# Optimization experiments

Hardware: AMD Instinct MI355X
Metric: run time of the kernel (lower is better)

The kernel has to match this reference:

```python
import jax, jax.numpy as jnp
import numpy as np

KER = 8

def _gelu(x):
    return jax.nn.gelu(x, approximate=False)

def _conv3x3(x, w, b):
    y = jax.lax.conv_general_dilated(x, w, (1, 1), 'SAME',
                                     dimension_numbers=('NCHW', 'OIHW', 'NCHW'))
    return y + b[None, :, None, None]

def _unfold(x):
    # F.unfold(kernel=8, stride=8): [B,C,H,W] -> [B, C*64, L], C-major then kh,kw
    B, C, H, W = x.shape
    Hb, Wb = H // KER, W // KER
    p = x.reshape(B, C, Hb, KER, Wb, KER).transpose(0, 1, 3, 5, 2, 4)
    return p.reshape(B, C * KER * KER, Hb * Wb)

def _fold(cols, H, W):
    # inverse of _unfold (non-overlapping patches)
    B, CK, L = cols.shape
    C = CK // (KER * KER)
    Hb, Wb = H // KER, W // KER
    p = cols.reshape(B, C, KER, KER, Hb, Wb).transpose(0, 1, 4, 2, 5, 3)
    return p.reshape(B, C, H, W)

def _bn(x, g, b, eps=1e-5):
    # train-mode BatchNorm1d on [B, C, L]: stats over (B, L) per channel
    m = x.mean(axis=(0, 2), keepdims=True)
    v = x.var(axis=(0, 2), keepdims=True)
    return (x - m) * jax.lax.rsqrt(v + eps) * g[None, :, None] + b[None, :, None]


def setup_inputs() -> dict:
    key = jax.random.key(0)
    ks = jax.random.split(key, 10)
    ind, d, hid = 64, 1024, 256
    f = lambda k, s: jax.random.normal(k, s, dtype=jnp.float32) * 0.02
    return {
        'feat': jax.random.normal(ks[0], (4, ind, 256, 256), dtype=jnp.float32),
        'w_enc': f(ks[1], (ind, ind, 3, 3)), 'b_enc': jnp.zeros((ind,), jnp.float32),
        'w_k': f(ks[2], (ind, ind, 3, 3)), 'b_k': jnp.zeros((ind,), jnp.float32),
        'w_v': f(ks[3], (ind, ind, 3, 3)), 'b_v': jnp.zeros((ind,), jnp.float32),
        'fcq_w': f(ks[4], (d, ind * KER * KER)), 'fcq_b': jnp.zeros((d,), jnp.float32),
        'fck_w': f(ks[5], (d, ind * KER * KER)), 'fck_b': jnp.zeros((d,), jnp.float32),
        'bnq_g': jnp.ones((d,), jnp.float32), 'bnq_b': jnp.zeros((d,), jnp.float32),
        'bnk_g': jnp.ones((d,), jnp.float32), 'bnk_b': jnp.zeros((d,), jnp.float32),
        'ff1_w': f(ks[6], (hid, ind)), 'ff1_b': jnp.zeros((hid,), jnp.float32),
        'ff2_w': f(ks[7], (ind, hid)), 'ff2_b': jnp.zeros((ind,), jnp.float32),
    }


def reference(feat, w_enc, b_enc, w_k, b_k, w_v, b_v,
              fcq_w, fcq_b, fck_w, fck_b, bnq_g, bnq_b, bnk_g, bnk_b,
              ff1_w, ff1_b, ff2_w, ff2_b):
    B, C, H, W = feat.shape
    fk = _gelu(_conv3x3(feat, w_k, b_k))
    fv = _gelu(_conv3x3(feat, w_v, b_v))
    refer = _gelu(_conv3x3(feat, w_enc, b_enc))
    q_un = _unfold(refer).transpose(0, 2, 1)   # [B, L, C*64]
    k_un = _unfold(fk).transpose(0, 2, 1)
    v_un = _unfold(fv).transpose(0, 2, 1)
    q = jnp.einsum('blc,dc->bld', q_un, fcq_w) + fcq_b
    q = _bn(q.transpose(0, 2, 1), bnq_g, bnq_b).transpose(0, 2, 1)  # [B, L, 1024]
    k = jnp.einsum('blc,dc->bld', k_un, fck_w) + fck_b
    k = _bn(k.transpose(0, 2, 1), bnk_g, bnk_b).transpose(0, 2, 1)
    scores = jnp.einsum('bld,bmd->blm', q, k) / jnp.sqrt(jnp.float32(q.shape[2]))
    attn = jax.nn.softmax(scores, axis=2)
    out = jnp.einsum('blm,bmc->blc', attn, v_un).transpose(0, 2, 1)  # [B, C*64, L]
    out = _fold(out, H, W)
    h = _gelu(jnp.einsum('bchw,oc->bohw', out, ff1_w) + ff1_b[None, :, None, None])
    h = _gelu(jnp.einsum('bchw,oc->bohw', h, ff2_w) + ff2_b[None, :, None, None])
    return h + feat
```

## Files before the change

### kernel.cpp

```cpp
#include <hip/hip_runtime.h>

typedef unsigned short u16;
typedef float f4 __attribute__((ext_vector_type(4)));
typedef float f32x4 __attribute__((ext_vector_type(4)));
typedef short bf16x8 __attribute__((ext_vector_type(8)));
typedef u16 u16x8 __attribute__((ext_vector_type(8)));
typedef u16 u16x4 __attribute__((ext_vector_type(4)));

__device__ __forceinline__ u16 f2bf(float f){
  unsigned u = __float_as_uint(f);
  u = (u + 0x7FFFu + ((u>>16)&1u)) >> 16;
  return (u16)u;
}
__device__ __forceinline__ float bf2f(u16 u){
  return __uint_as_float(((unsigned)u)<<16);
}
__device__ __forceinline__ float gelu_f(float x){
  float y = 1.5957691216057308f*(x + 0.044715f*x*x*x);
  y = fminf(y, 30.0f);
  float t = __expf(y);
  float r = __builtin_amdgcn_rcpf(t + 1.0f);
  return 0.5f*x*(1.0f + (t - 1.0f)*r);
}

typedef __attribute__((address_space(1))) const unsigned int as1_cuint;
typedef __attribute__((address_space(3))) unsigned int as3_uint;
__device__ __forceinline__ void gload_lds16(const void* g, void* l){
  __builtin_amdgcn_global_load_lds((as1_cuint*)g, (as3_uint*)l, 16, 0, 0);
}

__global__ __launch_bounds__(256) void to_nhwc(
    const float* __restrict__ F, u16* __restrict__ O)
{
  __shared__ float tile[64][65];
  const int t = threadIdx.x, b = blockIdx.y;
  const long px0 = (long)blockIdx.x*64;
  const float* Fb = F + (long)b*64*65536;
  #pragma unroll
  for (int i = 0; i < 4; ++i){
    const int ch = (t>>4) + i*16;
    const int pxo = (t&15)*4;
    f4 v = *(const f4*)&Fb[(long)ch*65536 + px0 + pxo];
    tile[ch][pxo]=v[0]; tile[ch][pxo+1]=v[1]; tile[ch][pxo+2]=v[2]; tile[ch][pxo+3]=v[3];
  }
  __syncthreads();
  const int px = t & 63, ch0 = (t>>6)*16;
  u16x8 o0, o1;
  #pragma unroll
  for (int j = 0; j < 8; ++j){ o0[j]=f2bf(tile[ch0+j][px]); o1[j]=f2bf(tile[ch0+8+j][px]); }
  u16* Ob = O + ((long)b*65536 + px0 + px)*64 + ch0;
  *(u16x8*)Ob = o0; *(u16x8*)(Ob+8) = o1;
}

__global__ __launch_bounds__(256) void wt_prep(
    const float* __restrict__ we, const float* __restrict__ wk,
    const float* __restrict__ wv, u16* __restrict__ Wt2)
{
  const int i = blockIdx.x*256 + threadIdx.x;
  const int cio = i & 31;
  const int t1 = i >> 5;
  const int n  = t1 % 192;
  const int t2 = t1 / 192;
  const int kc = t2 & 1, p = t2 >> 1;
  const int dy = p/3, dx = p - dy*3;
  const int ci = kc*32 + cio;
  const float* W = (n < 64) ? we : (n < 128) ? wk : wv;
  const int co = n & 63;
  Wt2[i] = f2bf(W[((co*64 + ci)*3 + dy)*3 + dx]);
}

__global__ __launch_bounds__(512,2) void conv_mfma(
    const u16* __restrict__ X, const u16* __restrict__ Wt2,
    const float* __restrict__ be, const float* __restrict__ bk, const float* __restrict__ bv,
    u16* __restrict__ Aq, u16* __restrict__ Ak, u16* __restrict__ Vl)
{
  __shared__ __align__(16) u16 smem[24576];
  const int t = threadIdx.x, lane = t & 63, wvi = t >> 6;
  const int bx = blockIdx.x, by = blockIdx.y, b = blockIdx.z;
  const int x0 = bx*16, y0 = by*8;
  const u16* Xb = X + (long)b*4194304;

  #pragma unroll
  for (int j = 0; j < 3; ++j){
    const int id = t + j*512;
    if (id < 1440){
      const int row = id / 144, rem = id - row*144, col = rem >> 3, ck = rem & 7;
      const int y = y0 - 1 + row, x = x0 - 1 + col;
      int4 v = {0,0,0,0};
      if ((unsigned)y < 256u && (unsigned)x < 256u)
        v = *(const int4*)(Xb + ((long)y*256 + x)*64 + ck*8);
      *(int4*)&smem[((row*18 + col)*8 + (ck ^ (col&7)))*8] = v;
    }
  }
  __syncthreads();

  const int wm4 = (wvi>>2)*4;
  const int wn  = (wvi&3)*48;
  const int fr = lane & 15, fo = lane >> 4;
  f32x4 acc[4][3] = {};

  #pragma unroll
  for (int dy = 0; dy < 3; ++dy)
  #pragma unroll
  for (int dx = 0; dx < 3; ++dx){
    const int p = dy*3 + dx;
    #pragma unroll
    for (int kc = 0; kc < 2; ++kc){
      bf16x8 af[4], bfv[3];
      const u16* wp = Wt2 + ((long)(p*2 + kc)*192 + wn + fr)*32 + fo*8;
      #pragma unroll
      for (int ni = 0; ni < 3; ++ni)
        bfv[ni] = *(const bf16x8*)(wp + ni*16*32);
      #pragma unroll
      for (int mi = 0; mi < 4; ++mi){
        const int row = wm4 + mi + dy;
        const int col = fr + dx;
        af[mi] = *(const bf16x8*)&smem[((row*18 + col)*8 + ((kc*4+fo) ^ (col&7)))*8];
      }
      #pragma unroll
      for (int mi = 0; mi < 4; ++mi)
        #pragma unroll
        for (int ni = 0; ni < 3; ++ni)
          acc[mi][ni] = __builtin_amdgcn_mfma_f32_16x16x32_bf16(af[mi], bfv[ni], acc[mi][ni], 0, 0, 0);
    }
  }
  __syncthreads();

  const int c0 = fo*4;
  const int lloc = c0 >> 3, kw0 = c0 & 7;
  #pragma unroll
  for (int ni = 0; ni < 3; ++ni){
    const int n = wn + ni*16 + fr;
    const int mat = n >> 6, co = n & 63;
    const float bias = (mat==0) ? be[co] : (mat==1) ? bk[co] : bv[co];
    #pragma unroll
    for (int mi = 0; mi < 4; ++mi){
      const int r = wm4 + mi;
      u16x4 o;
      #pragma unroll
      for (int rg = 0; rg < 4; ++rg) o[rg] = f2bf(gelu_f(acc[mi][ni][rg] + bias));
      const int e = ((mat*2 + lloc)*64 + co)*64 + ((r*8 + kw0) ^ ((co&7)<<3));
      *(u16x4*)&smem[e] = o;
    }
  }
  __syncthreads();

  const int l_lo = by*32 + bx*2;
  const int co_r = t >> 3, sw = (t&7) ^ (co_r&7);
  const int eoff = co_r*64 + sw*8;
  #pragma unroll
  for (int i = 0; i < 6; ++i){
    const int mat = i >> 1, ll = i & 1;
    u16x8 v = *(const u16x8*)&smem[(mat*2 + ll)*4096 + eoff];
    u16* dst = (mat==0 ? Aq : mat==1 ? Ak : Vl)
             + ((long)b*1024 + l_lo + ll)*4096 + t*8;
    *(u16x8*)dst = v;
  }
}

__global__ __launch_bounds__(256) void v_tr(
    const u16* __restrict__ S, u16* __restrict__ D)
{
  __shared__ u16 tl[64][72];
  const int t = threadIdx.x, b = blockIdx.z;
  const int ck0 = blockIdx.x*64, l0 = blockIdx.y*64;
  const u16* Sb = S + (long)b*4194304;
  u16* Db = D + (long)b*4194304;
  #pragma unroll
  for (int j = 0; j < 2; ++j){
    const int li = (t>>3) + j*32, cko = (t&7)*8;
    *(u16x8*)&tl[li][cko] = *(const u16x8*)(Sb + (long)(l0+li)*4096 + ck0 + cko);
  }
  __syncthreads();
  #pragma unroll
  for (int j = 0; j < 2; ++j){
    const int cki = (t>>3) + j*32, lo = (t&7)*8;
    u16x8 v;
    #pragma unroll
    for (int e = 0; e < 8; ++e) v[e] = tl[lo+e][cki];
    *(u16x8*)(Db + (long)(ck0+cki)*1024 + l0 + lo) = v;
  }
}

__device__ __forceinline__ void xcd_map(int gxl, int gyl, int n8l,
                                        int& bx, int& by, int& bz){
  const int s = blockIdx.x + (blockIdx.y<<gxl) + (blockIdx.z<<(gxl+gyl));
  const int orig = ((s & 7) << n8l) + (s >> 3);
  bx = orig & ((1<<gxl)-1);
  by = (orig >> gxl) & ((1<<gyl)-1);
  bz = orig >> (gxl+gyl);
}

__global__ __launch_bounds__(256,3) void gemm_av(
    const u16* __restrict__ A, long sA,
    const u16* __restrict__ B, long sB,
    void* __restrict__ Cv,
    const int M, const int N, const int K,
    const int gxl, const int gyl, const int n8l)
{
  int bx, by, bI;
  xcd_map(gxl, gyl, n8l, bx, by, bI);
  const u16* Ab = A + (long)bI*sA;
  const u16* Bb = B + (long)bI*sB;
  const int m0 = bx*128, n0 = by*128;
  __shared__ __align__(16) u16 As[8192];
  __shared__ __align__(16) u16 Bs[8192];
  const int t = threadIdx.x, lane = t & 63, wv = t >> 6;
  const int wm = (wv>>1)*64, wn = (wv&1)*64;
  const int fr = lane & 15, fo = lane >> 4;
  f32x4 acc[4][4] = {};
  const int c0 = wv*128 + lane, c1 = c0 + 64;
  const u16* Ag0 = Ab + (long)(m0 + (c0>>2))*K + (c0&3)*8;
  const u16* Ag1 = Ab + (long)(m0 + (c1>>2))*K + (c1&3)*8;
  const u16* Bg0 = Bb + (long)(n0 + (c0>>2))*K + (c0&3)*8;
  const u16* Bg1 = Bb + (long)(n0 + (c1>>2))*K + (c1&3)*8;
  const int lo0 = wv*1024;
  gload_lds16(Ag0, &As[lo0]);
  gload_lds16(Ag1, &As[lo0 + 512]);
  gload_lds16(Bg0, &Bs[lo0]);
  gload_lds16(Bg1, &Bs[lo0 + 512]);
  const int nk = K >> 5;
  int cur = 0;
  for (int ki = 0; ki < nk; ++ki){
    __syncthreads();
    if (ki + 1 < nk){
      const int k0 = (ki + 1) << 5;
      const int so = ((cur^1) << 12) + lo0;
      gload_lds16(Ag0 + k0, &As[so]);
      gload_lds16(Ag1 + k0, &As[so + 512]);
      gload_lds16(Bg0 + k0, &Bs[so]);
      gload_lds16(Bg1 + k0, &Bs[so + 512]);
    }
    const int ro = cur << 12;
    bf16x8 af[4], bfv[4];
    #pragma unroll
    for (int i = 0; i < 4; ++i){
      af[i]  = *(const bf16x8*)&As[ro + (wm + i*16 + fr)*32 + fo*8];
      bfv[i] = *(const bf16x8*)&Bs[ro + (wn + i*16 + fr)*32 + fo*8];
    }
    __builtin_amdgcn_s_setprio(1);
    #pragma unroll
    for (int mi = 0; mi < 4; ++mi)
      #pragma unroll
      for (int ni = 0; ni < 4; ++ni)
        acc[mi][ni] = __builtin_amdgcn_mfma_f32_16x16x32_bf16(af[mi], bfv[ni], acc[mi][ni], 0, 0, 0);
    __builtin_amdgcn_s_setprio(0);
    cur ^= 1;
  }
  u16* O = (u16*)Cv;
  #pragma unroll
  for (int mi = 0; mi < 4; ++mi)
    #pragma unroll
    for (int ni = 0; ni < 4; ++ni){
      const int col = n0 + wn + ni*16 + fr;
      const int c = col >> 6, khh = (col>>3)&7, kww = col&7;
      #pragma unroll
      for (int r = 0; r < 4; ++r){
        const int row = m0 + wm + mi*16 + fo*4 + r;
        const int hb = row >> 5, wbb = row & 31;
        O[(((long)bI*65536 + (hb*8+khh)*256 + wbb*8 + kww)<<6) + c] = f2bf(acc[mi][ni][r]);
      }
    }
}

template<int EPI>
__global__ __launch_bounds__(256,2) void gemm_bt128(
    const u16* __restrict__ A, long sA,
    const u16* __restrict__ B, long sB, const int zshB,
    void* __restrict__ Cv, long sC,
    const int M, const int N, const int K,
    float* __restrict__ bnstats,
    const int gxl, const int gyl, const int n8l)
{
  int bx, by, bI;
  xcd_map(gxl, gyl, n8l, bx, by, bI);
  const u16* Ab = A + (long)bI*sA;
  const u16* Bb = B + (long)(bI>>zshB)*sB;
  const int m0 = bx*128, n0 = by*128;
  __shared__ __align__(16) u16 As[16384];
  __shared__ __align__(16) u16 Bs[16384];
  const int t = threadIdx.x, lane = t & 63, wv = t >> 6;
  const int wm = (wv>>1)*64, wn = (wv&1)*64;
  const int fr = lane & 15, fo = lane >> 4;
  f32x4 acc[4][4] = {};
  const int c0 = wv*128 + lane, c1 = c0 + 64;
  const u16* Ag0 = Ab + (long)(m0 + (c0>>2))*K + (c0&3)*8;
  const u16* Ag1 = Ab + (long)(m0 + (c1>>2))*K + (c1&3)*8;
  const u16* Bg0 = Bb + (long)(n0 + (c0>>2))*K + (c0&3)*8;
  const u16* Bg1 = Bb + (long)(n0 + (c1>>2))*K + (c1&3)*8;
#define STAGEH(slot, h, kofs) { \
    u16* a_ = &As[(((slot)*2+(h))<<12) + wv*1024]; \
    u16* b_ = &Bs[(((slot)*2+(h))<<12) + wv*1024]; \
    const int ko_ = (kofs) + 32*(h); \
    gload_lds16(Ag0 + ko_, a_); \
    gload_lds16(Ag1 + ko_, a_ + 512); \
    gload_lds16(Bg0 + ko_, b_); \
    gload_lds16(Bg1 + ko_, b_ + 512); }
  STAGEH(0, 0, 0)
  STAGEH(0, 1, 0)
  const int nk = K >> 6;
  int cur = 0;
  for (int ki = 0; ki < nk; ++ki){
    __syncthreads();
    if (ki + 1 < nk){
      const int k0 = (ki + 1) << 6;
      STAGEH(cur^1, 0, k0)
      STAGEH(cur^1, 1, k0)
    }
    #pragma unroll
    for (int h = 0; h < 2; ++h){
      const int ro = ((cur*2 + h) << 12);
      bf16x8 af[4], bfv[4];
      #pragma unroll
      for (int i = 0; i < 4; ++i){
        af[i]  = *(const bf16x8*)&As[ro + (wm + i*16 + fr)*32 + fo*8];
        bfv[i] = *(const bf16x8*)&Bs[ro + (wn + i*16 + fr)*32 + fo*8];
      }
      __builtin_amdgcn_s_setprio(1);
      #pragma unroll
      for (int mi = 0; mi < 4; ++mi)
        #pragma unroll
        for (int ni = 0; ni < 4; ++ni)
          acc[mi][ni] = __builtin_amdgcn_mfma_f32_16x16x32_bf16(af[mi], bfv[ni], acc[mi][ni], 0, 0, 0);
      __builtin_amdgcn_s_setprio(0);
    }
    cur ^= 1;
  }
#undef STAGEH
  if (EPI == 0){
    float* Cf = (float*)Cv + (long)bI*sC;
    #pragma unroll
    for (int mi = 0; mi < 4; ++mi)
      #pragma unroll
      for (int ni = 0; ni < 4; ++ni){
        const int col = n0 + wn + ni*16 + fr;
        #pragma unroll
        for (int r = 0; r < 4; ++r){
          const int row = m0 + wm + mi*16 + fo*4 + r;
          Cf[(long)row*N + col] = acc[mi][ni][r];
        }
      }
  } else {
    u16* Cb = (u16*)Cv + (long)bI*sC;
    #pragma unroll
    for (int mi = 0; mi < 4; ++mi)
      #pragma unroll
      for (int ni = 0; ni < 4; ++ni){
        const int col = n0 + wn + ni*16 + fr;
        const int row0 = m0 + wm + mi*16 + fo*4;
        u16x4 o;
        #pragma unroll
        for (int r = 0; r < 4; ++r) o[r] = f2bf(acc[mi][ni][r]);
        *(u16x4*)&Cb[(long)col*M + row0] = o;
      }
    const int sel = bI >> 2;
    float* sums = bnstats + sel*2048;
    #pragma unroll
    for (int ni = 0; ni < 4; ++ni){
      float s = 0.f, q = 0.f;
      #pragma unroll
      for (int mi = 0; mi < 4; ++mi)
        #pragma unroll
        for (int r = 0; r < 4; ++r){
          const float v = acc[mi][ni][r];
          s += v; q += v*v;
        }
      s += __shfl_xor(s, 16); s += __shfl_xor(s, 32);
      q += __shfl_xor(q, 16); q += __shfl_xor(q, 32);
      if (fo == 0){
        const int col = n0 + wn + ni*16 + fr;
        atomicAdd(&sums[col], s);
        atomicAdd(&sums[1024 + col], q);
      }
    }
  }
}

__global__ __launch_bounds__(256,3) void ff1_mfma(
    const u16* __restrict__ X, const u16* __restrict__ W1b,
    const float* __restrict__ B1, u16* __restrict__ H1)
{
  const int t = threadIdx.x, lane = t & 63, wv = t >> 6;
  const long m0 = (long)blockIdx.x*128 + (wv>>1)*64;
  const int n0 = blockIdx.y*128 + (wv&1)*64;
  const int fr = lane & 15, fo = lane >> 4;
  f32x4 acc[4][4] = {};
  #pragma unroll
  for (int k0 = 0; k0 < 64; k0 += 32){
    bf16x8 af[4], bfv[4];
    #pragma unroll
    for (int i = 0; i < 4; ++i){
      af[i]  = *(const bf16x8*)(X   + (m0 + i*16 + fr)*64 + k0 + fo*8);
      bfv[i] = *(const bf16x8*)(W1b + (long)(n0 + i*16 + fr)*64 + k0 + fo*8);
    }
    #pragma unroll
    for (int mi = 0; mi < 4; ++mi)
      #pragma unroll
      for (int ni = 0; ni < 4; ++ni)
        acc[mi][ni] = __builtin_amdgcn_mfma_f32_16x16x32_bf16(af[mi], bfv[ni], acc[mi][ni], 0, 0, 0);
  }
  #pragma unroll
  for (int ni = 0; ni < 4; ++ni){
    const int col = n0 + ni*16 + fr;
    const float bc = B1[col];
    #pragma unroll
    for (int mi = 0; mi < 4; ++mi){
      const long row = m0 + mi*16 + fo*4;
      #pragma unroll
      for (int r = 0; r < 4; ++r)
        H1[(row + r)*256 + col] = f2bf(gelu_f(acc[mi][ni][r] + bc));
    }
  }
}

__global__ __launch_bounds__(256,3) void ff2_mfma(
    const u16* __restrict__ H1, const u16* __restrict__ W2b,
    const float* __restrict__ B2, const float* __restrict__ F,
    float* __restrict__ OUT)
{
  const int t = threadIdx.x, lane = t & 63, wv = t >> 6;
  const long m0 = (long)blockIdx.x*256 + wv*64;
  const int fr = lane & 15, fo = lane >> 4;
  f32x4 acc[4][4] = {};
  for (int k0 = 0; k0 < 256; k0 += 32){
    bf16x8 af[4], bfv[4];
    #pragma unroll
    for (int i = 0; i < 4; ++i){
      af[i]  = *(const bf16x8*)(H1  + (m0 + i*16 + fr)*256 + k0 + fo*8);
      bfv[i] = *(const bf16x8*)(W2b + (long)(i*16 + fr)*256 + k0 + fo*8);
    }
    #pragma unroll
    for (int mi = 0; mi < 4; ++mi)
      #pragma unroll
      for (int ni = 0; ni < 4; ++ni)
        acc[mi][ni] = __builtin_amdgcn_mfma_f32_16x16x32_bf16(af[mi], bfv[ni], acc[mi][ni], 0, 0, 0);
  }
  #pragma unroll
  for (int ni = 0; ni < 4; ++ni){
    const int c = ni*16 + fr;
    const float bc = B2[c];
    #pragma unroll
    for (int mi = 0; mi < 4; ++mi){
      const long p = m0 + mi*16 + fo*4;
      const int b = (int)(p >> 16), pp = (int)(p & 65535);
      const long idx = ((long)(b*64 + c))*65536 + pp;
      const f4 fres = *(const f4*)&F[idx];
      f4 o;
      #pragma unroll
      for (int r = 0; r < 4; ++r) o[r] = gelu_f(acc[mi][ni][r] + bc) + fres[r];
      *(f4*)&OUT[idx] = o;
    }
  }
}

__global__ __launch_bounds__(256) void cvt_w(
    const float* __restrict__ Wq, const float* __restrict__ Wk,
    u16* __restrict__ Oq, u16* __restrict__ Ok)
{
  const long i = ((long)blockIdx.x*256 + threadIdx.x)*4;
  const float* s = blockIdx.y ? Wk : Wq;
  u16* d = blockIdx.y ? Ok : Oq;
  f4 v = *(const f4*)&s[i];
  u16x4 o; o[0]=f2bf(v[0]); o[1]=f2bf(v[1]); o[2]=f2bf(v[2]); o[3]=f2bf(v[3]);
  *(u16x4*)&d[i] = o;
}

__global__ __launch_bounds__(256) void cvt_ffw(
    const float* __restrict__ W1, const float* __restrict__ W2,
    u16* __restrict__ O1, u16* __restrict__ O2)
{
  const long i = ((long)blockIdx.x*256 + threadIdx.x)*4;
  const float* s = blockIdx.y ? W2 : W1;
  u16* d = blockIdx.y ? O2 : O1;
  f4 v = *(const f4*)&s[i];
  u16x4 o; o[0]=f2bf(v[0]); o[1]=f2bf(v[1]); o[2]=f2bf(v[2]); o[3]=f2bf(v[3]);
  *(u16x4*)&d[i] = o;
}

__global__ void bn_fin2(float* __restrict__ stats,
                        const float* __restrict__ gq, const float* __restrict__ bq,
                        const float* __restrict__ gk, const float* __restrict__ bk)
{
  const int sel = blockIdx.y;
  const int d = blockIdx.x*256 + threadIdx.x;
  if (d >= 1024) return;
  const float* sum   = stats + sel*2048;
  const float* sumsq = sum + 1024;
  const float* g    = sel ? gk : gq;
  const float* beta = sel ? bk : bq;
  const float m  = sum[d]   * (1.f/4096.f);
  const float vv = sumsq[d] * (1.f/4096.f) - m*m;
  const float sc = g[d] * rsqrtf(vv + 1e-5f);
  stats[4096 + sel*2048 + d]        = sc;
  stats[4096 + sel*2048 + 1024 + d] = beta[d] - m*sc;
}

__global__ __launch_bounds__(256) void bn_apply_t(
    const u16* __restrict__ QT, const float* __restrict__ stats,
    u16* __restrict__ Y)
{
  __shared__ u16 tl[64][72];
  const int t = threadIdx.x, zi = blockIdx.z;
  const int d0 = blockIdx.x*64, l0 = blockIdx.y*64;
  const int sel = zi >> 2;
  const u16* S = QT + (long)zi*1048576;
  u16* D = Y + (long)zi*1048576;
  const float* scp = stats + 4096 + sel*2048;
  const float* shp = scp + 1024;
  #pragma unroll
  for (int j = 0; j < 2; ++j){
    const int di = (t>>3) + j*32, lo = (t&7)*8;
    const int d = d0 + di;
    const float sc = scp[d], sh = shp[d];
    u16x8 v = *(const u16x8*)(S + (long)d*1024 + l0 + lo);
    u16x8 o;
    #pragma unroll
    for (int e = 0; e < 8; ++e) o[e] = f2bf(bf2f(v[e])*sc + sh);
    *(u16x8*)&tl[di][lo] = o;
  }
  __syncthreads();
  #pragma unroll
  for (int j = 0; j < 2; ++j){
    const int li = (t>>3) + j*32, dof = (t&7)*8;
    u16x8 v;
    #pragma unroll
    for (int e = 0; e < 8; ++e) v[e] = tl[dof+e][li];
    *(u16x8*)(D + (long)(l0+li)*1024 + d0 + dof) = v;
  }
}

__global__ __launch_bounds__(256) void softmax_k(
    const float* __restrict__ S, u16* __restrict__ P)
{
  const long row = blockIdx.x;
  const float* p = S + row*1024;
  const int t = threadIdx.x;
  f4 v = *(const f4*)&p[t*4];
  v *= 0.03125f;
  float mx = fmaxf(fmaxf(v[0],v[1]), fmaxf(v[2],v[3]));
  #pragma unroll
  for (int o = 1; o < 64; o <<= 1) mx = fmaxf(mx, __shfl_xor(mx, o));
  __shared__ float red[4], red2[4];
  if ((t & 63) == 0) red[t>>6] = mx;
  __syncthreads();
  mx = fmaxf(fmaxf(red[0],red[1]), fmaxf(red[2],red[3]));
  f4 e;
  e[0]=__expf(v[0]-mx); e[1]=__expf(v[1]-mx); e[2]=__expf(v[2]-mx); e[3]=__expf(v[3]-mx);
  float sm = e[0]+e[1]+e[2]+e[3];
  #pragma unroll
  for (int o = 1; o < 64; o <<= 1) sm += __shfl_xor(sm, o);
  if ((t & 63) == 0) red2[t>>6] = sm;
  __syncthreads();
  sm = red2[0]+red2[1]+red2[2]+red2[3];
  const float inv = 1.0f/sm;
  u16x4 o4; o4[0]=f2bf(e[0]*inv); o4[1]=f2bf(e[1]*inv); o4[2]=f2bf(e[2]*inv); o4[3]=f2bf(e[3]*inv);
  *(u16x4*)&P[row*1024 + t*4] = o4;
}

extern "C" void kernel_launch(void* const* d_in, const int* in_sizes, int n_in,
                              void* d_out, int out_size, void* d_ws, size_t ws_size,
                              hipStream_t stream)
{
  const float* feat  = (const float*)d_in[0];
  const float* w_enc = (const float*)d_in[1];
  const float* b_enc = (const float*)d_in[2];
  const float* w_k   = (const float*)d_in[3];
  const float* b_k   = (const float*)d_in[4];
  const float* w_v   = (const float*)d_in[5];
  const float* b_v   = (const float*)d_in[6];
  const float* fcq_w = (const float*)d_in[7];
  const float* fck_w = (const float*)d_in[9];
  const float* bnq_g = (const float*)d_in[11];
  const float* bnq_b = (const float*)d_in[12];
  const float* bnk_g = (const float*)d_in[13];
  const float* bnk_b = (const float*)d_in[14];
  const float* ff1w  = (const float*)d_in[15];
  const float* ff1b  = (const float*)d_in[16];
  const float* ff2w  = (const float*)d_in[17];
  const float* ff2b  = (const float*)d_in[18];

  char* ws = (char*)d_ws;
  u16*   Aq      = (u16*)  (ws);
  u16*   Ak      = (u16*)  (ws + (32ull<<20));
  u16*   Vc      = (u16*)  (ws + (64ull<<20));
  u16*   Wq      = (u16*)  (ws + (96ull<<20));
  u16*   Wk      = (u16*)  (ws + (104ull<<20));
  u16*   q_bf    = (u16*)  (ws + (112ull<<20));
  u16*   k_bf    = (u16*)  (ws + (120ull<<20));
  u16*   qk_rawT = (u16*)  (ws + (128ull<<20));
  float* scores  = (float*)(ws + (160ull<<20));
  u16*   attn    = (u16*)  (ws + (176ull<<20));
  u16*   out_nhwc= (u16*)  (ws + (184ull<<20));
  u16*   NX      = (u16*)  (ws + (128ull<<20));
  u16*   Vl      = (u16*)  (ws + (160ull<<20));
  u16*   Wt2     = (u16*)  (ws + (216ull<<20));
  float* stats   = (float*)(ws + (217ull<<20));
  u16*   W1b     = (u16*)  (ws + (218ull<<20));
  u16*   W2b     = (u16*)  (ws + (218ull<<20) + 65536);
  u16*   h1      = (u16*)  (ws);

  hipMemsetAsync(stats, 0, 4096*sizeof(float), stream);

  to_nhwc<<<dim3(1024,4), 256, 0, stream>>>(feat, NX);
  wt_prep<<<dim3(432), 256, 0, stream>>>(w_enc, w_k, w_v, Wt2);
  conv_mfma<<<dim3(16,32,4), 512, 0, stream>>>(NX, Wt2, b_enc, b_k, b_v, Aq, Ak, Vl);
  v_tr<<<dim3(64,16,4), 256, 0, stream>>>(Vl, Vc);
  cvt_w<<<dim3(4096,2), 256, 0, stream>>>(fcq_w, fck_w, Wq, Wk);
  cvt_ffw<<<dim3(16,2), 256, 0, stream>>>(ff1w, ff2w, W1b, W2b);

  gemm_bt128<2><<<dim3(8,8,8), 256, 0, stream>>>(Aq, 4194304, Wq, 4194304, 2,
                                                 qk_rawT, 1048576, 1024, 1024, 4096, stats,
                                                 3, 3, 6);

  bn_fin2<<<dim3(4,2), 256, 0, stream>>>(stats, bnq_g, bnq_b, bnk_g, bnk_b);
  bn_apply_t<<<dim3(16,16,8), 256, 0, stream>>>(qk_rawT, stats, q_bf);

  gemm_bt128<0><<<dim3(8,8,4), 256, 0, stream>>>(q_bf, 1048576, k_bf, 1048576, 0,
                                                 scores, 1048576, 1024, 1024, 1024, nullptr,
                                                 3, 3, 5);
  softmax_k<<<dim3(4096), 256, 0, stream>>>(scores, attn);

  gemm_av<<<dim3(8,32,4), 256, 0, stream>>>(attn, 1048576, Vc, 4194304,
                                            out_nhwc, 1024, 4096, 1024,
                                            3, 5, 7);

  ff1_mfma<<<dim3(2048,2), 256, 0, stream>>>(out_nhwc, W1b, ff1b, h1);
  ff2_mfma<<<dim3(1024), 256, 0, stream>>>(h1, W2b, ff2b, feat, (float*)d_out);
}
```

Measured before the change: 515.4 us.

## Fuse the two feed-forward GEMMs through a shared-memory hidden tile

Merges the ff1 and ff2 kernels into one. Each block computes a 128x256 GELU hidden tile into LDS, then runs the second GEMM from LDS with the residual add. This removes the global write and read of the 128MB bf16 hidden activation and one launch. In exchange it uses a large LDS allocation, which limits occupancy, and higher register use.

```diff
diff --git a/kernel.cpp b/kernel.cpp
--- a/kernel.cpp
+++ b/kernel.cpp
@@ -376,79 +376,82 @@
   }
 }
 
-__global__ __launch_bounds__(256,3) void ff1_mfma(
+__global__ __launch_bounds__(256,2) void ff_fused(
     const u16* __restrict__ X, const u16* __restrict__ W1b,
-    const float* __restrict__ B1, u16* __restrict__ H1)
-{
-  const int t = threadIdx.x, lane = t & 63, wv = t >> 6;
-  const long m0 = (long)blockIdx.x*128 + (wv>>1)*64;
-  const int n0 = blockIdx.y*128 + (wv&1)*64;
-  const int fr = lane & 15, fo = lane >> 4;
-  f32x4 acc[4][4] = {};
-  #pragma unroll
-  for (int k0 = 0; k0 < 64; k0 += 32){
-    bf16x8 af[4], bfv[4];
-    #pragma unroll
-    for (int i = 0; i < 4; ++i){
-      af[i]  = *(const bf16x8*)(X   + (m0 + i*16 + fr)*64 + k0 + fo*8);
-      bfv[i] = *(const bf16x8*)(W1b + (long)(n0 + i*16 + fr)*64 + k0 + fo*8);
-    }
-    #pragma unroll
-    for (int mi = 0; mi < 4; ++mi)
-      #pragma unroll
-      for (int ni = 0; ni < 4; ++ni)
-        acc[mi][ni] = __builtin_amdgcn_mfma_f32_16x16x32_bf16(af[mi], bfv[ni], acc[mi][ni], 0, 0, 0);
-  }
-  #pragma unroll
-  for (int ni = 0; ni < 4; ++ni){
-    const int col = n0 + ni*16 + fr;
-    const float bc = B1[col];
-    #pragma unroll
-    for (int mi = 0; mi < 4; ++mi){
-      const long row = m0 + mi*16 + fo*4;
-      #pragma unroll
-      for (int r = 0; r < 4; ++r)
-        H1[(row + r)*256 + col] = f2bf(gelu_f(acc[mi][ni][r] + bc));
-    }
-  }
-}
-
-__global__ __launch_bounds__(256,3) void ff2_mfma(
-    const u16* __restrict__ H1, const u16* __restrict__ W2b,
+    const float* __restrict__ B1, const u16* __restrict__ W2b,
     const float* __restrict__ B2, const float* __restrict__ F,
     float* __restrict__ OUT)
 {
+  __shared__ __align__(16) u16 h1s[128*264];
   const int t = threadIdx.x, lane = t & 63, wv = t >> 6;
-  const long m0 = (long)blockIdx.x*256 + wv*64;
+  const long m0 = (long)blockIdx.x*128;
   const int fr = lane & 15, fo = lane >> 4;
-  f32x4 acc[4][4] = {};
-  for (int k0 = 0; k0 < 256; k0 += 32){
-    bf16x8 af[4], bfv[4];
-    #pragma unroll
-    for (int i = 0; i < 4; ++i){
-      af[i]  = *(const bf16x8*)(H1  + (m0 + i*16 + fr)*256 + k0 + fo*8);
-      bfv[i] = *(const bf16x8*)(W2b + (long)(i*16 + fr)*256 + k0 + fo*8);
-    }
-    #pragma unroll
-    for (int mi = 0; mi < 4; ++mi)
+
+  {
+    const int wm = (wv>>1)*64, wn = (wv&1)*128;
+    f32x4 acc[4][8] = {};
+    #pragma unroll
+    for (int kc = 0; kc < 2; ++kc){
+      bf16x8 af[4], bf[8];
+      #pragma unroll
+      for (int mi = 0; mi < 4; ++mi)
+        af[mi] = *(const bf16x8*)(X + (m0 + wm + mi*16 + fr)*64 + kc*32 + fo*8);
+      #pragma unroll
+      for (int ni = 0; ni < 8; ++ni)
+        bf[ni] = *(const bf16x8*)(W1b + (long)(wn + ni*16 + fr)*64 + kc*32 + fo*8);
+      #pragma unroll
+      for (int mi = 0; mi < 4; ++mi)
+        #pragma unroll
+        for (int ni = 0; ni < 8; ++ni)
+          acc[mi][ni] = __builtin_amdgcn_mfma_f32_16x16x32_bf16(af[mi], bf[ni], acc[mi][ni], 0, 0, 0);
+    }
+    #pragma unroll
+    for (int ni = 0; ni < 8; ++ni){
+      const int col = wn + ni*16 + fr;
+      const float bc = B1[col];
+      #pragma unroll
+      for (int mi = 0; mi < 4; ++mi){
+        const int row0 = wm + mi*16 + fo*4;
+        #pragma unroll
+        for (int r = 0; r < 4; ++r)
+          h1s[(row0 + r)*264 + col] = f2bf(gelu_f(acc[mi][ni][r] + bc));
+      }
+    }
+  }
+  __syncthreads();
+
+  {
+    const int wm2 = wv*32;
+    f32x4 acc2[2][4] = {};
+    for (int k0 = 0; k0 < 256; k0 += 32){
+      bf16x8 af2[2], bf2[4];
+      #pragma unroll
+      for (int mi = 0; mi < 2; ++mi)
+        af2[mi] = *(const bf16x8*)&h1s[(wm2 + mi*16 + fr)*264 + k0 + fo*8];
       #pragma unroll
       for (int ni = 0; ni < 4; ++ni)
-        acc[mi][ni] = __builtin_amdgcn_mfma_f32_16x16x32_bf16(af[mi], bfv[ni], acc[mi][ni], 0, 0, 0);
-  }
-  #pragma unroll
-  for (int ni = 0; ni < 4; ++ni){
-    const int c = ni*16 + fr;
-    const float bc = B2[c];
-    #pragma unroll
-    for (int mi = 0; mi < 4; ++mi){
-      const long p = m0 + mi*16 + fo*4;
-      const int b = (int)(p >> 16), pp = (int)(p & 65535);
-      const long idx = ((long)(b*64 + c))*65536 + pp;
-      const f4 fres = *(const f4*)&F[idx];
-      f4 o;
-      #pragma unroll
-      for (int r = 0; r < 4; ++r) o[r] = gelu_f(acc[mi][ni][r] + bc) + fres[r];
-      *(f4*)&OUT[idx] = o;
+        bf2[ni] = *(const bf16x8*)(W2b + (long)(ni*16 + fr)*256 + k0 + fo*8);
+      #pragma unroll
+      for (int mi = 0; mi < 2; ++mi)
+        #pragma unroll
+        for (int ni = 0; ni < 4; ++ni)
+          acc2[mi][ni] = __builtin_amdgcn_mfma_f32_16x16x32_bf16(af2[mi], bf2[ni], acc2[mi][ni], 0, 0, 0);
+    }
+    #pragma unroll
+    for (int ni = 0; ni < 4; ++ni){
+      const int c = ni*16 + fr;
+      const float bc = B2[c];
+      #pragma unroll
+      for (int mi = 0; mi < 2; ++mi){
+        const long p = m0 + wm2 + mi*16 + fo*4;
+        const int b = (int)(p >> 16), pp = (int)(p & 65535);
+        const long idx = ((long)(b*64 + c))*65536 + pp;
+        const f4 fres = *(const f4*)&F[idx];
+        f4 o;
+        #pragma unroll
+        for (int r = 0; r < 4; ++r) o[r] = gelu_f(acc2[mi][ni][r] + bc) + fres[r];
+        *(f4*)&OUT[idx] = o;
+      }
     }
   }
 }
@@ -597,7 +600,6 @@
   float* stats   = (float*)(ws + (217ull<<20));
   u16*   W1b     = (u16*)  (ws + (218ull<<20));
   u16*   W2b     = (u16*)  (ws + (218ull<<20) + 65536);
-  u16*   h1      = (u16*)  (ws);
 
   hipMemsetAsync(stats, 0, 4096*sizeof(float), stream);
 
@@ -624,6 +626,6 @@
                                             out_nhwc, 1024, 4096, 1024,
                                             3, 5, 7);
 
-  ff1_mfma<<<dim3(2048,2), 256, 0, stream>>>(out_nhwc, W1b, ff1b, h1);
-  ff2_mfma<<<dim3(1024), 256, 0, stream>>>(h1, W2b, ff2b, feat, (float*)d_out);
-}
+  ff_fused<<<dim3(2048), 256, 0, stream>>>(out_nhwc, W1b, ff1b, W2b, ff2b,
+                                           feat, (float*)d_out);
+}
```

Result: faster. 477.9 us (-7.3%).
